# Kernel optimization log

Hardware: AMD Instinct MI355X
Metric: run time of the kernel (lower is better)

Reference implementation:

```python
import jax, jax.numpy as jnp
import numpy as np

B, L, D, H = 2, 128, 256, 256
BASE_LR = 0.01
LR_SHIFT = float(np.log(np.expm1(BASE_LR)))  # log(expm1(base_lr))


def silu_backward(x):
    s = jax.nn.silu(x)
    return s + jax.nn.sigmoid(x) * (1.0 - s)


def decay_matrix(log_g):
    # log_g: [B,L] -> M[b,l,m] = exp(sum_{i=m+1..l} log_g[b,i]) for m<=l, else 0
    n = log_g.shape[1]
    strict = jnp.tril(jnp.ones((n, n), log_g.dtype), -1)
    cum = jnp.cumsum(log_g[:, :, None] * strict, axis=1)
    return jnp.exp(cum) * jnp.tril(jnp.ones((n, n), log_g.dtype))


def setup_inputs():
    key = jax.random.key(0)
    ks = jax.random.split(key, 22)
    p = lambda k, shape: jax.random.normal(k, shape, jnp.float32) * 0.02
    inp = {
        'x': jax.random.normal(ks[0], (B, L, D), jnp.float32),
        'Wq': p(ks[1], (D, D)), 'bq': p(ks[2], (D,)),
        'Wk': p(ks[3], (D, D)), 'bk': p(ks[4], (D,)),
        'Wv': p(ks[5], (D, D)), 'bv': p(ks[6], (D,)),
        'Wlr': p(ks[7], (D, 1)), 'blr': p(ks[8], (1,)),
        'Wm': p(ks[9], (D, 1)), 'bm': p(ks[10], (1,)),
        'Wd': p(ks[11], (D, 1)), 'bd': p(ks[12], (1,)),
        'W1': p(ks[13], (B, H, D)), 'b1': p(ks[14], (B, H)),
        'W2': p(ks[15], (B, D, H)), 'b2': p(ks[16], (B, D)),
        'mW1': p(ks[17], (B, H, D)), 'mb1': p(ks[18], (B, H)),
        'mW2': p(ks[19], (B, D, H)), 'mb2': p(ks[20], (B, D)),
    }
    return inp


def reference(x, Wq, bq, Wk, bk, Wv, bv, Wlr, blr, Wm, bm, Wd, bd,
              W1, b1, W2, b2, mW1, mb1, mW2, mb2):
    query = x @ Wq + bq
    key_ = x @ Wk + bk
    value = x @ Wv + bv

    # forward through fast-weight MLP at current (chunk-start) weights
    Z1 = jnp.einsum('bhd,bld->blh', W1, key_) + b1[:, None, :]
    X2 = jax.nn.silu(Z1)
    Z2 = jnp.einsum('bdh,blh->bld', W2, X2) + b2[:, None, :]

    # per-token gradients of 0.5*||Z2 - value||^2
    grad_Z2 = Z2 - value
    grad_b2 = grad_Z2
    grad_W2 = jnp.einsum('bld,blh->bldh', grad_Z2, X2)
    grad_X2 = jnp.einsum('bld,bdh->blh', grad_Z2, W2)
    grad_Z1 = grad_X2 * silu_backward(Z1)
    grad_b1 = grad_Z1
    grad_W1 = jnp.einsum('blh,bld->blhd', grad_Z1, key_)

    lr = jax.nn.softplus((x @ Wlr).squeeze(-1) + blr + LR_SHIFT)  # [B,L]
    gW1 = grad_W1 * lr[:, :, None, None]
    gb1 = grad_b1 * lr[:, :, None]
    gW2 = grad_W2 * lr[:, :, None, None]
    gb2 = grad_b2 * lr[:, :, None]

    # momentum recurrence (decay-gated linear scan, materialized as LxL matrix)
    fc_mom = (x @ Wm).squeeze(-1) + bm  # [B,L]
    log_mom = -jax.nn.softplus(-fc_mom)
    M = decay_matrix(log_mom)  # [B,L,L]
    mom_cum = jnp.exp(jnp.cumsum(log_mom, axis=1))  # [B,L]

    mgW1 = jnp.einsum('blm,bmhd->blhd', M, gW1) - jnp.einsum('bl,bhd->blhd', mom_cum, mW1)
    mgb1 = jnp.einsum('blm,bmh->blh', M, gb1) - jnp.einsum('bl,bh->blh', mom_cum, mb1)
    mgW2 = jnp.einsum('blm,bmdh->bldh', M, gW2) - jnp.einsum('bl,bdh->bldh', mom_cum, mW2)
    mgb2 = jnp.einsum('blm,bmd->bld', M, gb2) - jnp.einsum('bl,bd->bld', mom_cum, mb2)

    # weight-decay recurrence
    log_wd = -jax.nn.softplus((x @ Wd).squeeze(-1) + bd)  # [B,L]
    Dm = decay_matrix(log_wd)
    wd_cum = jnp.exp(jnp.cumsum(log_wd, axis=1))

    W1p = jnp.einsum('blm,bmhd->blhd', Dm, mgW1) + jnp.einsum('bl,bhd->blhd', wd_cum, W1)
    b1p = jnp.einsum('blm,bmh->blh', Dm, mgb1) + jnp.einsum('bl,bh->blh', wd_cum, b1)
    W2p = jnp.einsum('blm,bmdh->bldh', Dm, mgW2) + jnp.einsum('bl,bdh->bldh', wd_cum, W2)
    b2p = jnp.einsum('blm,bmd->bld', Dm, mgb2) + jnp.einsum('bl,bd->bld', wd_cum, b2)

    # query pass through per-token updated weights
    Zq1 = jnp.einsum('blhd,bld->blh', W1p, query) + b1p
    Zq2 = jnp.einsum('bldh,blh->bld', W2p, jax.nn.silu(Zq1)) + b2p

    return (Zq2,
            W1p[:, -1], b1p[:, -1], W2p[:, -1], b2p[:, -1],
            mgW1[:, -1], mgb1[:, -1], mgW2[:, -1], mgb2[:, -1])
```

## Files before the change

kernel.cpp:

```cpp
#include <hip/hip_runtime.h>
#include <math.h>

constexpr int Bn = 2, Ln = 128, Dn = 256, Hn = 256;

#define LR_SHIFT (-4.6001660040607144f)

constexpr int OFF_Q      = 0;
constexpr int OFF_K      = 65536;
constexpr int OFF_V      = 131072;
constexpr int OFF_X2     = 196608;
constexpr int OFF_GZ1    = 262144;
constexpr int OFF_GZ2    = 327680;
constexpr int OFF_XQ     = 393216;
constexpr int OFF_KT     = 458752;
constexpr int OFF_A      = 524288;
constexpr int OFF_W1T    = 557056;
constexpr int OFF_W2T    = 688128;
constexpr int OFF_MW1T   = 819200;
constexpr int OFF_MW2T   = 950272;
constexpr int OFF_LR     = 1081344;
constexpr int OFF_PM     = 1081600;
constexpr int OFF_PD     = 1081856;
constexpr int OFF_MOMCUM = 1082112;
constexpr int OFF_WDCUM  = 1082368;
constexpr int OFF_C      = 1082624;
constexpr int OFF_LOGM   = 1082880;
constexpr int OFF_LOGWD  = 1083136;
constexpr int OFF_X2T    = 1083392;
constexpr int OFF_U1     = 1148928;
constexpr int OFF_V1     = 1214464;
constexpr int OFF_U2     = 1280000;
constexpr int OFF_V2     = 1345536;
constexpr int OFF_P1     = 1411072;
constexpr int OFF_P2     = OFF_V;

constexpr int OUT_ZQ2  = 0;
constexpr int OUT_W1P  = 65536;
constexpr int OUT_B1P  = 196608;
constexpr int OUT_W2P  = 197120;
constexpr int OUT_B2P  = 328192;
constexpr int OUT_MGW1 = 328704;
constexpr int OUT_MGB1 = 459776;
constexpr int OUT_MGW2 = 460288;
constexpr int OUT_MGB2 = 591360;

struct KParams {
    const float *x;
    const float *Wq, *bq, *Wk, *bk, *Wv, *bv;
    const float *Wlr, *blr, *Wm, *bm, *Wd, *bd;
    const float *W1, *b1, *W2, *b2, *mW1, *mb1, *mW2, *mb2;
    float *out, *ws;
};

__device__ __forceinline__ float softplus_f(float z) {
    return fmaxf(z, 0.0f) + log1pf(expf(-fabsf(z)));
}
__device__ __forceinline__ float4 fma4(float s, const float4 w, float4 a) {
    a.x += s * w.x; a.y += s * w.y; a.z += s * w.z; a.w += s * w.w; return a;
}
__device__ __forceinline__ float silu_f(float z) {
    return z / (1.0f + expf(-z));
}
__device__ __forceinline__ float dsilu_mul(float a, float z) {
    float sg = 1.0f / (1.0f + expf(-z));
    return a * (sg * (1.0f + z * (1.0f - sg)));
}

__device__ __forceinline__ void stage8(const float* __restrict__ src,
                                       float (*xs)[260], int t) {
#pragma unroll
    for (int i = 0; i < 2; ++i) {
        int e = t + i * 256; int tok = e >> 6, kq = e & 63;
        *(float4*)&xs[tok][kq * 4] = *(const float4*)(src + tok * 256 + kq * 4);
    }
}

__device__ __forceinline__ float4 dot256(const float (*xs)[260], int tok,
                                         const float* __restrict__ Wc, int ldw) {
    float4 a = {0, 0, 0, 0};
    for (int k0 = 0; k0 < 256; k0 += 32) {
        float4 wb[32];
#pragma unroll
        for (int kk = 0; kk < 32; ++kk)
            wb[kk] = *(const float4*)(Wc + (k0 + kk) * ldw);
#pragma unroll
        for (int kk = 0; kk < 32; ++kk)
            a = fma4(xs[tok][k0 + kk], wb[kk], a);
    }
    return a;
}

__device__ __forceinline__ void lastw_unit(const KParams& p, float* smem, int t,
                                           int b, int fam, int i0, int j0) {
    const float* ws = p.ws;
    float* wa = smem;
    float* wm = smem + 128;
    float (*LA)[16] = (float (*)[16])(smem + 256);
    float (*LM)[16] = (float (*)[16])(smem + 256 + 2048);
    float (*R)[16]  = (float (*)[16])(smem + 256 + 4096);
    const float* lr = ws + OFF_LR + b * Ln;
    const float* Pm = ws + OFF_PM + b * Ln;
    const float* Arow = ws + OFF_A + (b * Ln + Ln - 1) * Ln;
    if (t < 128) {
        wa[t] = Arow[t] * lr[t];
        wm[t] = expf(Pm[Ln - 1] - Pm[t]) * lr[t];
    }
    const float* left  = ws + (fam == 0 ? OFF_GZ1 : OFF_GZ2) + b * Ln * 256;
    const float* right = ws + (fam == 0 ? OFF_K   : OFF_X2 ) + b * Ln * 256;
    __syncthreads();
#pragma unroll
    for (int i = 0; i < 2; ++i) {
        int e = t + i * 256;
        int m = e >> 2, iq = (e & 3) * 4;
        float4 lv = *(const float4*)(left + m * 256 + i0 + iq);
        float4 rv = *(const float4*)(right + m * 256 + j0 + iq);
        float wam = wa[m], wmm = wm[m];
        LA[m][iq + 0] = wam * lv.x; LA[m][iq + 1] = wam * lv.y;
        LA[m][iq + 2] = wam * lv.z; LA[m][iq + 3] = wam * lv.w;
        LM[m][iq + 0] = wmm * lv.x; LM[m][iq + 1] = wmm * lv.y;
        LM[m][iq + 2] = wmm * lv.z; LM[m][iq + 3] = wmm * lv.w;
        R[m][iq + 0] = rv.x; R[m][iq + 1] = rv.y;
        R[m][iq + 2] = rv.z; R[m][iq + 3] = rv.w;
    }
    __syncthreads();
    int tx = t & 15, ty = t >> 4;
    float accA = 0.0f, accM = 0.0f;
#pragma unroll 4
    for (int m = 0; m < 128; ++m) {
        accA += LA[m][ty] * R[m][tx];
        accM += LM[m][ty] * R[m][tx];
    }
    float c_last  = ws[OFF_C + b * Ln + Ln - 1];
    float wd_last = ws[OFF_WDCUM + b * Ln + Ln - 1];
    float mc_last = ws[OFF_MOMCUM + b * Ln + Ln - 1];
    int i = i0 + ty, j = j0 + tx;
    const float* base1 = (fam == 0 ? p.W1 : p.W2) + b * 65536;
    const float* basem = (fam == 0 ? p.mW1 : p.mW2) + b * 65536;
    float b1v = base1[i * 256 + j], bmv = basem[i * 256 + j];
    int op = (fam == 0 ? OUT_W1P : OUT_W2P) + (b * 256 + i) * 256 + j;
    int om = (fam == 0 ? OUT_MGW1 : OUT_MGW2) + (b * 256 + i) * 256 + j;
    p.out[op] = accA - c_last * bmv + wd_last * b1v;
    p.out[om] = accM - mc_last * bmv;
}

__device__ __forceinline__ void score_unit(const KParams& p, float* smem, int t,
                                           int b, int l0, int srcoff, int btoff,
                                           int poff) {
    const float* ws = p.ws;
    float (*qs)[260] = (float (*)[260])smem;
    stage8(ws + srcoff + (b * 128 + l0) * 256, qs, t);
    __syncthreads();
    int tok = t >> 5, mq = t & 31, m0 = 4 * mq;
    int l = l0 + tok;
    float4 s = dot256(qs, tok, ws + btoff + b * 32768 + m0, 128);
    float4 A4 = *(const float4*)(ws + OFF_A + (b * 128 + l) * 128 + m0);
    float4 L4 = *(const float4*)(ws + OFF_LR + b * 128 + m0);
    float4 pv;
    pv.x = (m0 + 0 <= l) ? A4.x * L4.x * (1.0f + s.x) : 0.0f;
    pv.y = (m0 + 1 <= l) ? A4.y * L4.y * (1.0f + s.y) : 0.0f;
    pv.z = (m0 + 2 <= l) ? A4.z * L4.z * (1.0f + s.z) : 0.0f;
    pv.w = (m0 + 3 <= l) ? A4.w * L4.w * (1.0f + s.w) : 0.0f;
    *(float4*)(p.ws + poff + b * 16384 + l * 128 + m0) = pv;
}

__device__ __forceinline__ void combine_unit(const KParams& p, float* smem, int t,
                                             int b, int l0, int c0, int poff,
                                             int goff, int uoff, int voff,
                                             int dooutsilu, float* dst) {
    const float* ws = p.ws;
    int bl0 = b * 128 + l0;
    float (*ps)[132] = (float (*)[132])smem;
    {
        int tok = t >> 5, mq = t & 31;
        *(float4*)&ps[tok][mq * 4] =
            *(const float4*)(ws + poff + b * 16384 + (l0 + tok) * 128 + mq * 4);
    }
    __syncthreads();
    int tok = t >> 5, q = t & 31;
    int l = l0 + tok;
    int c = c0 + 4 * q;
    float cl  = ws[OFF_C + b * 128 + l];
    float wdc = ws[OFF_WDCUM + b * 128 + l];
    float4 acc = {0, 0, 0, 0};
    const float* G = ws + goff + b * 32768 + c;
    int mmax = l0 + 8;
    int m0 = 0;
    for (; m0 + 16 <= mmax; m0 += 16) {
        float4 gb[16];
#pragma unroll
        for (int kk = 0; kk < 16; ++kk)
            gb[kk] = *(const float4*)(G + (m0 + kk) * 256);
#pragma unroll
        for (int kk = 0; kk < 16; ++kk)
            acc = fma4(ps[tok][m0 + kk], gb[kk], acc);
    }
    for (; m0 < mmax; m0 += 8) {
        float4 gb[8];
#pragma unroll
        for (int kk = 0; kk < 8; ++kk)
            gb[kk] = *(const float4*)(G + (m0 + kk) * 256);
#pragma unroll
        for (int kk = 0; kk < 8; ++kk)
            acc = fma4(ps[tok][m0 + kk], gb[kk], acc);
    }
    float4 u4 = *(const float4*)(ws + uoff + (bl0 + tok) * 256 + c);
    float4 v4 = *(const float4*)(ws + voff + (bl0 + tok) * 256 + c);
    float4 o;
    o.x = acc.x - cl * v4.x + wdc * u4.x;
    o.y = acc.y - cl * v4.y + wdc * u4.y;
    o.z = acc.z - cl * v4.z + wdc * u4.z;
    o.w = acc.w - cl * v4.w + wdc * u4.w;
    if (dooutsilu) {
        o.x = silu_f(o.x); o.y = silu_f(o.y); o.z = silu_f(o.z); o.w = silu_f(o.w);
    }
    *(float4*)(dst + (bl0 + tok) * 256 + c) = o;
}

__global__ __launch_bounds__(256) void phase0_kernel(KParams p) {
    __shared__ float smem[4160];
    int u = blockIdx.x, t = threadIdx.x;
    float* ws = p.ws;
    if (u < 512) {
        int z = u >> 6; int mat = z >> 1; int b = z & 1;
        const float* src; float* dst;
        if (mat == 0)      { src = p.W1  + b * 65536; dst = ws + OFF_W1T  + b * 65536; }
        else if (mat == 1) { src = p.W2  + b * 65536; dst = ws + OFF_W2T  + b * 65536; }
        else if (mat == 2) { src = p.mW1 + b * 65536; dst = ws + OFF_MW1T + b * 65536; }
        else               { src = p.mW2 + b * 65536; dst = ws + OFF_MW2T + b * 65536; }
        float (*tile)[33] = (float (*)[33])smem;
        int tx = t & 31, ty = t >> 5;
        int tid = u & 63;
        int r0 = (tid >> 3) * 32, c0 = (tid & 7) * 32;
        for (int i = 0; i < 32; i += 8)
            tile[ty + i][tx] = src[(r0 + ty + i) * 256 + (c0 + tx)];
        __syncthreads();
        for (int i = 0; i < 32; i += 8)
            dst[(c0 + ty + i) * 256 + (r0 + tx)] = tile[tx][ty + i];
    } else if (u < 704) {
        int v = u - 512; int mat = v >> 6; int r = v & 63;
        int ct = r >> 5, tt = r & 31;
        int bl0 = tt * 8, c0 = ct * 128;
        const float* W    = (mat == 0) ? p.Wq : (mat == 1) ? p.Wk : p.Wv;
        const float* bias = (mat == 0) ? p.bq : (mat == 1) ? p.bk : p.bv;
        int outoff = (mat == 0) ? OFF_Q : (mat == 1) ? OFF_K : OFF_V;
        float (*xs)[260] = (float (*)[260])smem;
        stage8(p.x + bl0 * 256, xs, t);
        __syncthreads();
        int tok = t >> 5, q = t & 31;
        int c = c0 + 4 * q;
        float4 a = dot256(xs, tok, W + c, 256);
        float4 bb = *(const float4*)(bias + c);
        a.x += bb.x; a.y += bb.y; a.z += bb.z; a.w += bb.w;
        *(float4*)(ws + outoff + (bl0 + tok) * 256 + c) = a;
        if (mat == 1) {
            int b = bl0 >> 7, l = (bl0 & 127) + tok;
            float* KT = ws + OFF_KT + b * 32768 + l;
            KT[(c + 0) * 128] = a.x; KT[(c + 1) * 128] = a.y;
            KT[(c + 2) * 128] = a.z; KT[(c + 3) * 128] = a.w;
        }
    } else {
        int blk = u - 704;
        int ln = t & 63, wv = t >> 6;
        int bl = blk * 4 + wv;
        float4 xv = *(const float4*)(p.x + bl * 256 + ln * 4);
        float4 wl = *(const float4*)(p.Wlr + ln * 4);
        float4 wm = *(const float4*)(p.Wm + ln * 4);
        float4 wd = *(const float4*)(p.Wd + ln * 4);
        float s1 = xv.x * wl.x + xv.y * wl.y + xv.z * wl.z + xv.w * wl.w;
        float s2 = xv.x * wm.x + xv.y * wm.y + xv.z * wm.z + xv.w * wm.w;
        float s3 = xv.x * wd.x + xv.y * wd.y + xv.z * wd.z + xv.w * wd.w;
#pragma unroll
        for (int off = 32; off > 0; off >>= 1) {
            s1 += __shfl_xor(s1, off);
            s2 += __shfl_xor(s2, off);
            s3 += __shfl_xor(s3, off);
        }
        if (ln == 0) {
            ws[OFF_LR + bl]    = softplus_f(s1 + p.blr[0] + LR_SHIFT);
            ws[OFF_LOGM + bl]  = -softplus_f(-(s2 + p.bm[0]));
            ws[OFF_LOGWD + bl] = -softplus_f(s3 + p.bd[0]);
        }
    }
}

__global__ __launch_bounds__(256) void phase1_kernel(KParams p) {
    __shared__ float smem[4160];
    int u = blockIdx.x, t = threadIdx.x;
    float* ws = p.ws;
    if (u < 64) {
        int tt = u >> 1, ct = u & 1;
        int bl0 = tt * 8, c0 = ct * 128, b = bl0 >> 7;
        float (*xs)[260] = (float (*)[260])smem;
        stage8(ws + OFF_K + bl0 * 256, xs, t);
        __syncthreads();
        int tok = t >> 5, q = t & 31;
        int c = c0 + 4 * q;
        float4 a = dot256(xs, tok, ws + OFF_W1T + b * 65536 + c, 256);
        float4 bb = *(const float4*)(p.b1 + b * 256 + c);
        float4 z = {a.x + bb.x, a.y + bb.y, a.z + bb.z, a.w + bb.w};
        *(float4*)(ws + OFF_GZ1 + (bl0 + tok) * 256 + c) = z;
        float4 s = {silu_f(z.x), silu_f(z.y), silu_f(z.z), silu_f(z.w)};
        *(float4*)(ws + OFF_X2 + (bl0 + tok) * 256 + c) = s;
        int l = (bl0 & 127) + tok;
        float* X2T = ws + OFF_X2T + b * 32768 + l;
        X2T[(c + 0) * 128] = s.x; X2T[(c + 1) * 128] = s.y;
        X2T[(c + 2) * 128] = s.z; X2T[(c + 3) * 128] = s.w;
    } else if (u < 320) {
        int w = u - 64; int b = w >> 7; int l = w & 127;
        float* sm = smem;
        float* sd = smem + 128;
        float* se = smem + 256;
        if (t < 128) {
            sm[t] = ws[OFF_LOGM + b * Ln + t];
            sd[t] = ws[OFF_LOGWD + b * Ln + t];
        }
        __syncthreads();
        for (int off = 1; off < 128; off <<= 1) {
            float am = 0.0f, ad = 0.0f;
            if (t < 128 && t >= off) { am = sm[t - off]; ad = sd[t - off]; }
            __syncthreads();
            if (t < 128) { sm[t] += am; sd[t] += ad; }
            __syncthreads();
        }
        if (l == 0) {
            if (t < 128) {
                float pm = sm[t], pd = sd[t];
                ws[OFF_PM + b * Ln + t] = pm;
                ws[OFF_PD + b * Ln + t] = pd;
                ws[OFF_MOMCUM + b * Ln + t] = expf(pm);
                ws[OFF_WDCUM + b * Ln + t]  = expf(pd);
                se[t] = expf(pm - pd);
            }
            __syncthreads();
            for (int off = 1; off < 128; off <<= 1) {
                float a = 0.0f;
                if (t < 128 && t >= off) a = se[t - off];
                __syncthreads();
                if (t < 128) se[t] += a;
                __syncthreads();
            }
            if (t < 128) ws[OFF_C + b * Ln + t] = expf(sd[t]) * se[t];
        }
        if (t < 128) {
            int m1 = t;
            float a = 0.0f;
            if (m1 <= l) {
                float pdl = sd[l], pmm1 = sm[m1];
                float s = 0.0f;
                for (int m = m1; m <= l; ++m)
                    s += expf((pdl - sd[m]) + (sm[m] - pmm1));
                a = s;
            }
            ws[OFF_A + (b * Ln + l) * Ln + m1] = a;
        }
    } else {
        int w = u - 320; int mat = w >> 6; int r = w & 63;
        int tt = r >> 1, ct = r & 1;
        int bl0 = tt * 8, c0 = ct * 128, b = bl0 >> 7;
        float (*xs)[260] = (float (*)[260])smem;
        stage8(ws + OFF_Q + bl0 * 256, xs, t);
        __syncthreads();
        int tok = t >> 5, q = t & 31;
        int c = c0 + 4 * q;
        const float* W = ws + (mat ? OFF_MW1T : OFF_W1T) + b * 65536 + c;
        const float* bias = (mat ? p.mb1 : p.b1) + b * 256 + c;
        float4 a = dot256(xs, tok, W, 256);
        float4 bb = *(const float4*)bias;
        a.x += bb.x; a.y += bb.y; a.z += bb.z; a.w += bb.w;
        *(float4*)(ws + (mat ? OFF_V1 : OFF_U1) + (bl0 + tok) * 256 + c) = a;
    }
}

__global__ __launch_bounds__(256) void phase2_kernel(KParams p) {
    __shared__ float smem[4160];
    int u = blockIdx.x, t = threadIdx.x;
    float* ws = p.ws;
    if (u < 64) {
        int tt = u >> 1, ct = u & 1;
        int bl0 = tt * 8, c0 = ct * 128, b = bl0 >> 7;
        float (*xs)[260] = (float (*)[260])smem;
        stage8(ws + OFF_X2 + bl0 * 256, xs, t);
        __syncthreads();
        int tok = t >> 5, q = t & 31;
        int c = c0 + 4 * q;
        float4 a = dot256(xs, tok, ws + OFF_W2T + b * 65536 + c, 256);
        float4 bb = *(const float4*)(p.b2 + b * 256 + c);
        float4 v4 = *(const float4*)(ws + OFF_V + (bl0 + tok) * 256 + c);
        float4 g = {a.x + bb.x - v4.x, a.y + bb.y - v4.y,
                    a.z + bb.z - v4.z, a.w + bb.w - v4.w};
        *(float4*)(ws + OFF_GZ2 + (bl0 + tok) * 256 + c) = g;
    } else {
        int w = u - 64; int b = w >> 4; int l0 = (w & 15) * 8;
        score_unit(p, smem, t, b, l0, OFF_Q, OFF_KT, OFF_P1);
    }
}

__global__ __launch_bounds__(256) void phase3_kernel(KParams p) {
    __shared__ float smem[6400];
    int u = blockIdx.x, t = threadIdx.x;
    float* ws = p.ws;
    if (u < 64) {
        int tt = u >> 1, ct = u & 1;
        int bl0 = tt * 8, c0 = ct * 128, b = bl0 >> 7;
        float (*xs)[260] = (float (*)[260])smem;
        stage8(ws + OFF_GZ2 + bl0 * 256, xs, t);
        __syncthreads();
        int tok = t >> 5, q = t & 31;
        int c = c0 + 4 * q;
        float4 a = dot256(xs, tok, p.W2 + b * 65536 + c, 256);
        float4 z = *(const float4*)(ws + OFF_GZ1 + (bl0 + tok) * 256 + c);
        float4 g = {dsilu_mul(a.x, z.x), dsilu_mul(a.y, z.y),
                    dsilu_mul(a.z, z.z), dsilu_mul(a.w, z.w)};
        *(float4*)(ws + OFF_GZ1 + (bl0 + tok) * 256 + c) = g;
    } else {
        int w = u - 64; int b = w >> 8; int rem = w & 255;
        lastw_unit(p, smem, t, b, 1, (rem >> 4) * 16, (rem & 15) * 16);
    }
}

__global__ __launch_bounds__(256) void phase4_kernel(KParams p) {
    __shared__ float smem[6400];
    int u = blockIdx.x, t = threadIdx.x;
    float* ws = p.ws;
    if (u < 64) {
        int tt = u >> 1, ct = u & 1;
        int b = tt >> 4, l0 = (tt & 15) * 8;
        combine_unit(p, smem, t, b, l0, ct * 128, OFF_P1, OFF_GZ1,
                     OFF_U1, OFF_V1, 1, ws + OFF_XQ);
    } else if (u < 576) {
        int w = u - 64; int b = w >> 8; int rem = w & 255;
        lastw_unit(p, smem, t, b, 0, (rem >> 4) * 16, (rem & 15) * 16);
    } else {
        int b = u - 576;
        float* wa = smem;
        float* wm = smem + 128;
        if (t < 128) {
            wa[t] = ws[OFF_A + (b * Ln + Ln - 1) * Ln + t] * ws[OFF_LR + b * Ln + t];
            wm[t] = expf(ws[OFF_PM + b * Ln + Ln - 1] - ws[OFF_PM + b * Ln + t]) *
                    ws[OFF_LR + b * Ln + t];
        }
        __syncthreads();
        const float* gz1 = ws + OFF_GZ1 + b * Ln * 256;
        const float* gz2 = ws + OFF_GZ2 + b * Ln * 256;
        float sA1 = 0, sM1 = 0, sA2 = 0, sM2 = 0;
        for (int m0 = 0; m0 < 128; m0 += 16) {
            float g1b[16], g2b[16];
#pragma unroll
            for (int kk = 0; kk < 16; ++kk) {
                g1b[kk] = gz1[(m0 + kk) * 256 + t];
                g2b[kk] = gz2[(m0 + kk) * 256 + t];
            }
#pragma unroll
            for (int kk = 0; kk < 16; ++kk) {
                float wam = wa[m0 + kk], wmm = wm[m0 + kk];
                sA1 += wam * g1b[kk]; sM1 += wmm * g1b[kk];
                sA2 += wam * g2b[kk]; sM2 += wmm * g2b[kk];
            }
        }
        float c_last  = ws[OFF_C + b * Ln + Ln - 1];
        float wd_last = ws[OFF_WDCUM + b * Ln + Ln - 1];
        float mc_last = ws[OFF_MOMCUM + b * Ln + Ln - 1];
        p.out[OUT_B1P + b * 256 + t]  = sA1 - c_last * p.mb1[b * 256 + t] + wd_last * p.b1[b * 256 + t];
        p.out[OUT_MGB1 + b * 256 + t] = sM1 - mc_last * p.mb1[b * 256 + t];
        p.out[OUT_B2P + b * 256 + t]  = sA2 - c_last * p.mb2[b * 256 + t] + wd_last * p.b2[b * 256 + t];
        p.out[OUT_MGB2 + b * 256 + t] = sM2 - mc_last * p.mb2[b * 256 + t];
    }
}

__global__ __launch_bounds__(256) void phase5_kernel(KParams p) {
    __shared__ float smem[4160];
    int u = blockIdx.x, t = threadIdx.x;
    float* ws = p.ws;
    if (u < 32) {
        int b = u >> 4; int l0 = (u & 15) * 8;
        score_unit(p, smem, t, b, l0, OFF_XQ, OFF_X2T, OFF_P2);
    } else {
        int w = u - 32; int mat = w >> 6; int r = w & 63;
        int tt = r >> 1, ct = r & 1;
        int bl0 = tt * 8, c0 = ct * 128, b = bl0 >> 7;
        float (*xs)[260] = (float (*)[260])smem;
        stage8(ws + OFF_XQ + bl0 * 256, xs, t);
        __syncthreads();
        int tok = t >> 5, q = t & 31;
        int c = c0 + 4 * q;
        const float* W = ws + (mat ? OFF_MW2T : OFF_W2T) + b * 65536 + c;
        const float* bias = (mat ? p.mb2 : p.b2) + b * 256 + c;
        float4 a = dot256(xs, tok, W, 256);
        float4 bb = *(const float4*)bias;
        a.x += bb.x; a.y += bb.y; a.z += bb.z; a.w += bb.w;
        *(float4*)(ws + (mat ? OFF_V2 : OFF_U2) + (bl0 + tok) * 256 + c) = a;
    }
}

__global__ __launch_bounds__(256) void phase6_kernel(KParams p) {
    __shared__ float smem[1056];
    int u = blockIdx.x, t = threadIdx.x;
    int tt = u >> 1, ct = u & 1;
    int b = tt >> 4, l0 = (tt & 15) * 8;
    combine_unit(p, smem, t, b, l0, ct * 128, OFF_P2, OFF_GZ2,
                 OFF_U2, OFF_V2, 0, p.out + OUT_ZQ2);
}

extern "C" void kernel_launch(void* const* d_in, const int* in_sizes, int n_in,
                              void* d_out, int out_size, void* d_ws, size_t ws_size,
                              hipStream_t stream) {
    KParams p;
    p.x   = (const float*)d_in[0];
    p.Wq  = (const float*)d_in[1];  p.bq  = (const float*)d_in[2];
    p.Wk  = (const float*)d_in[3];  p.bk  = (const float*)d_in[4];
    p.Wv  = (const float*)d_in[5];  p.bv  = (const float*)d_in[6];
    p.Wlr = (const float*)d_in[7];  p.blr = (const float*)d_in[8];
    p.Wm  = (const float*)d_in[9];  p.bm  = (const float*)d_in[10];
    p.Wd  = (const float*)d_in[11]; p.bd  = (const float*)d_in[12];
    p.W1  = (const float*)d_in[13]; p.b1  = (const float*)d_in[14];
    p.W2  = (const float*)d_in[15]; p.b2  = (const float*)d_in[16];
    p.mW1 = (const float*)d_in[17]; p.mb1 = (const float*)d_in[18];
    p.mW2 = (const float*)d_in[19]; p.mb2 = (const float*)d_in[20];
    p.out = (float*)d_out;
    p.ws  = (float*)d_ws;

    phase0_kernel<<<768, 256, 0, stream>>>(p);
    phase1_kernel<<<448, 256, 0, stream>>>(p);
    phase2_kernel<<<96, 256, 0, stream>>>(p);
    phase3_kernel<<<576, 256, 0, stream>>>(p);
    phase4_kernel<<<578, 256, 0, stream>>>(p);
    phase5_kernel<<<160, 256, 0, stream>>>(p);
    phase6_kernel<<<64, 256, 0, stream>>>(p);
}
```

Before: 234.0 us.

## Fuse backward and query-pass phases into fewer kernels, cut launches from seven to four

Merges the grad_Z2 and grad_Z1 computations into one block per 8-token tile, keeping grad_Z2 in shared memory. It also fuses the query-side combine, score, U2/V2 projections and final output into a single per-tile path, which removes the U2/V2/P2 workspace round-trips. That path runs inside the same launch as the last-weight reductions, so two launches and several global-memory passes disappear. The dot256 prefetch batch shrinks from 32 to 16 float4 registers to offset the higher register pressure. The trade-off is fewer blocks for the serial per-tile work, so each block does much more sequential computation.

```diff
diff --git a/kernel.cpp b/kernel.cpp
--- a/kernel.cpp
+++ b/kernel.cpp
@@ -29,10 +29,7 @@
 constexpr int OFF_X2T    = 1083392;
 constexpr int OFF_U1     = 1148928;
 constexpr int OFF_V1     = 1214464;
-constexpr int OFF_U2     = 1280000;
-constexpr int OFF_V2     = 1345536;
 constexpr int OFF_P1     = 1411072;
-constexpr int OFF_P2     = OFF_V;
 
 constexpr int OUT_ZQ2  = 0;
 constexpr int OUT_W1P  = 65536;
@@ -78,13 +75,13 @@
 __device__ __forceinline__ float4 dot256(const float (*xs)[260], int tok,
                                          const float* __restrict__ Wc, int ldw) {
     float4 a = {0, 0, 0, 0};
-    for (int k0 = 0; k0 < 256; k0 += 32) {
-        float4 wb[32];
-#pragma unroll
-        for (int kk = 0; kk < 32; ++kk)
+    for (int k0 = 0; k0 < 256; k0 += 16) {
+        float4 wb[16];
+#pragma unroll
+        for (int kk = 0; kk < 16; ++kk)
             wb[kk] = *(const float4*)(Wc + (k0 + kk) * ldw);
 #pragma unroll
-        for (int kk = 0; kk < 32; ++kk)
+        for (int kk = 0; kk < 16; ++kk)
             a = fma4(xs[tok][k0 + kk], wb[kk], a);
     }
     return a;
@@ -163,27 +160,10 @@
     *(float4*)(p.ws + poff + b * 16384 + l * 128 + m0) = pv;
 }
 
-__device__ __forceinline__ void combine_unit(const KParams& p, float* smem, int t,
-                                             int b, int l0, int c0, int poff,
-                                             int goff, int uoff, int voff,
-                                             int dooutsilu, float* dst) {
-    const float* ws = p.ws;
-    int bl0 = b * 128 + l0;
-    float (*ps)[132] = (float (*)[132])smem;
-    {
-        int tok = t >> 5, mq = t & 31;
-        *(float4*)&ps[tok][mq * 4] =
-            *(const float4*)(ws + poff + b * 16384 + (l0 + tok) * 128 + mq * 4);
-    }
-    __syncthreads();
-    int tok = t >> 5, q = t & 31;
-    int l = l0 + tok;
-    int c = c0 + 4 * q;
-    float cl  = ws[OFF_C + b * 128 + l];
-    float wdc = ws[OFF_WDCUM + b * 128 + l];
+__device__ __forceinline__ float4 pg_dot(const float* __restrict__ G,
+                                         const float* __restrict__ prow,
+                                         int mmax) {
     float4 acc = {0, 0, 0, 0};
-    const float* G = ws + goff + b * 32768 + c;
-    int mmax = l0 + 8;
     int m0 = 0;
     for (; m0 + 16 <= mmax; m0 += 16) {
         float4 gb[16];
@@ -192,7 +172,7 @@
             gb[kk] = *(const float4*)(G + (m0 + kk) * 256);
 #pragma unroll
         for (int kk = 0; kk < 16; ++kk)
-            acc = fma4(ps[tok][m0 + kk], gb[kk], acc);
+            acc = fma4(prow[m0 + kk], gb[kk], acc);
     }
     for (; m0 < mmax; m0 += 8) {
         float4 gb[8];
@@ -201,19 +181,9 @@
             gb[kk] = *(const float4*)(G + (m0 + kk) * 256);
 #pragma unroll
         for (int kk = 0; kk < 8; ++kk)
-            acc = fma4(ps[tok][m0 + kk], gb[kk], acc);
-    }
-    float4 u4 = *(const float4*)(ws + uoff + (bl0 + tok) * 256 + c);
-    float4 v4 = *(const float4*)(ws + voff + (bl0 + tok) * 256 + c);
-    float4 o;
-    o.x = acc.x - cl * v4.x + wdc * u4.x;
-    o.y = acc.y - cl * v4.y + wdc * u4.y;
-    o.z = acc.z - cl * v4.z + wdc * u4.z;
-    o.w = acc.w - cl * v4.w + wdc * u4.w;
-    if (dooutsilu) {
-        o.x = silu_f(o.x); o.y = silu_f(o.y); o.z = silu_f(o.z); o.w = silu_f(o.w);
-    }
-    *(float4*)(dst + (bl0 + tok) * 256 + c) = o;
+            acc = fma4(prow[m0 + kk], gb[kk], acc);
+    }
+    return acc;
 }
 
 __global__ __launch_bounds__(256) void phase0_kernel(KParams p) {
@@ -375,22 +345,47 @@
     __shared__ float smem[4160];
     int u = blockIdx.x, t = threadIdx.x;
     float* ws = p.ws;
-    if (u < 64) {
-        int tt = u >> 1, ct = u & 1;
-        int bl0 = tt * 8, c0 = ct * 128, b = bl0 >> 7;
+    if (u < 32) {
+        int bl0 = u * 8, b = bl0 >> 7;
         float (*xs)[260] = (float (*)[260])smem;
+        float (*gs)[260] = (float (*)[260])(smem + 2080);
         stage8(ws + OFF_X2 + bl0 * 256, xs, t);
         __syncthreads();
         int tok = t >> 5, q = t & 31;
-        int c = c0 + 4 * q;
-        float4 a = dot256(xs, tok, ws + OFF_W2T + b * 65536 + c, 256);
-        float4 bb = *(const float4*)(p.b2 + b * 256 + c);
-        float4 v4 = *(const float4*)(ws + OFF_V + (bl0 + tok) * 256 + c);
-        float4 g = {a.x + bb.x - v4.x, a.y + bb.y - v4.y,
-                    a.z + bb.z - v4.z, a.w + bb.w - v4.w};
-        *(float4*)(ws + OFF_GZ2 + (bl0 + tok) * 256 + c) = g;
+        int c = 4 * q, c2 = c + 128;
+        {
+            const float* W2t = ws + OFF_W2T + b * 65536;
+            float4 a0 = dot256(xs, tok, W2t + c, 256);
+            float4 a1 = dot256(xs, tok, W2t + c2, 256);
+            float4 bb0 = *(const float4*)(p.b2 + b * 256 + c);
+            float4 bb1 = *(const float4*)(p.b2 + b * 256 + c2);
+            float4 v0 = *(const float4*)(ws + OFF_V + (bl0 + tok) * 256 + c);
+            float4 v1 = *(const float4*)(ws + OFF_V + (bl0 + tok) * 256 + c2);
+            float4 g0 = {a0.x + bb0.x - v0.x, a0.y + bb0.y - v0.y,
+                         a0.z + bb0.z - v0.z, a0.w + bb0.w - v0.w};
+            float4 g1 = {a1.x + bb1.x - v1.x, a1.y + bb1.y - v1.y,
+                         a1.z + bb1.z - v1.z, a1.w + bb1.w - v1.w};
+            *(float4*)&gs[tok][c]  = g0;
+            *(float4*)&gs[tok][c2] = g1;
+            *(float4*)(ws + OFF_GZ2 + (bl0 + tok) * 256 + c)  = g0;
+            *(float4*)(ws + OFF_GZ2 + (bl0 + tok) * 256 + c2) = g1;
+        }
+        __syncthreads();
+        {
+            const float* W2n = p.W2 + b * 65536;
+            float4 a0 = dot256(gs, tok, W2n + c, 256);
+            float4 a1 = dot256(gs, tok, W2n + c2, 256);
+            float4 z0 = *(const float4*)(ws + OFF_GZ1 + (bl0 + tok) * 256 + c);
+            float4 z1 = *(const float4*)(ws + OFF_GZ1 + (bl0 + tok) * 256 + c2);
+            float4 g0 = {dsilu_mul(a0.x, z0.x), dsilu_mul(a0.y, z0.y),
+                         dsilu_mul(a0.z, z0.z), dsilu_mul(a0.w, z0.w)};
+            float4 g1 = {dsilu_mul(a1.x, z1.x), dsilu_mul(a1.y, z1.y),
+                         dsilu_mul(a1.z, z1.z), dsilu_mul(a1.w, z1.w)};
+            *(float4*)(ws + OFF_GZ1 + (bl0 + tok) * 256 + c)  = g0;
+            *(float4*)(ws + OFF_GZ1 + (bl0 + tok) * 256 + c2) = g1;
+        }
     } else {
-        int w = u - 64; int b = w >> 4; int l0 = (w & 15) * 8;
+        int w = u - 32; int b = w >> 4; int l0 = (w & 15) * 8;
         score_unit(p, smem, t, b, l0, OFF_Q, OFF_KT, OFF_P1);
     }
 }
@@ -399,39 +394,71 @@
     __shared__ float smem[6400];
     int u = blockIdx.x, t = threadIdx.x;
     float* ws = p.ws;
-    if (u < 64) {
-        int tt = u >> 1, ct = u & 1;
-        int bl0 = tt * 8, c0 = ct * 128, b = bl0 >> 7;
-        float (*xs)[260] = (float (*)[260])smem;
-        stage8(ws + OFF_GZ2 + bl0 * 256, xs, t);
+    if (u < 32) {
+        int b = u >> 4; int l0 = (u & 15) * 8; int bl0 = b * 128 + l0;
+        float (*xqs)[260] = (float (*)[260])smem;
+        float (*ps)[132]  = (float (*)[132])(smem + 2080);
+        {
+            int tok = t >> 5, mq = t & 31;
+            *(float4*)&ps[tok][mq * 4] =
+                *(const float4*)(ws + OFF_P1 + b * 16384 + (l0 + tok) * 128 + mq * 4);
+        }
         __syncthreads();
         int tok = t >> 5, q = t & 31;
-        int c = c0 + 4 * q;
-        float4 a = dot256(xs, tok, p.W2 + b * 65536 + c, 256);
-        float4 z = *(const float4*)(ws + OFF_GZ1 + (bl0 + tok) * 256 + c);
-        float4 g = {dsilu_mul(a.x, z.x), dsilu_mul(a.y, z.y),
-                    dsilu_mul(a.z, z.z), dsilu_mul(a.w, z.w)};
-        *(float4*)(ws + OFF_GZ1 + (bl0 + tok) * 256 + c) = g;
+        int l = l0 + tok;
+        float cl  = ws[OFF_C + b * 128 + l];
+        float wdc = ws[OFF_WDCUM + b * 128 + l];
+        int mmax = l0 + 8;
+#pragma unroll
+        for (int half = 0; half < 2; ++half) {
+            int c = half * 128 + 4 * q;
+            float4 acc = pg_dot(ws + OFF_GZ1 + b * 32768 + c, ps[tok], mmax);
+            float4 u4 = *(const float4*)(ws + OFF_U1 + (bl0 + tok) * 256 + c);
+            float4 v4 = *(const float4*)(ws + OFF_V1 + (bl0 + tok) * 256 + c);
+            float4 o;
+            o.x = silu_f(acc.x - cl * v4.x + wdc * u4.x);
+            o.y = silu_f(acc.y - cl * v4.y + wdc * u4.y);
+            o.z = silu_f(acc.z - cl * v4.z + wdc * u4.z);
+            o.w = silu_f(acc.w - cl * v4.w + wdc * u4.w);
+            *(float4*)&xqs[tok][c] = o;
+        }
+        __syncthreads();
+        {
+            int mq = t & 31, m0 = 4 * mq;
+            float4 s = dot256(xqs, tok, ws + OFF_X2T + b * 32768 + m0, 128);
+            float4 A4 = *(const float4*)(ws + OFF_A + (b * 128 + l) * 128 + m0);
+            float4 L4 = *(const float4*)(ws + OFF_LR + b * 128 + m0);
+            float4 pv;
+            pv.x = (m0 + 0 <= l) ? A4.x * L4.x * (1.0f + s.x) : 0.0f;
+            pv.y = (m0 + 1 <= l) ? A4.y * L4.y * (1.0f + s.y) : 0.0f;
+            pv.z = (m0 + 2 <= l) ? A4.z * L4.z * (1.0f + s.z) : 0.0f;
+            pv.w = (m0 + 3 <= l) ? A4.w * L4.w * (1.0f + s.w) : 0.0f;
+            *(float4*)&ps[tok][m0] = pv;
+        }
+        __syncthreads();
+#pragma unroll
+        for (int half = 0; half < 2; ++half) {
+            int c = half * 128 + 4 * q;
+            float4 uacc = dot256(xqs, tok, ws + OFF_W2T + b * 65536 + c, 256);
+            float4 bb = *(const float4*)(p.b2 + b * 256 + c);
+            uacc.x += bb.x; uacc.y += bb.y; uacc.z += bb.z; uacc.w += bb.w;
+            float4 vacc = dot256(xqs, tok, ws + OFF_MW2T + b * 65536 + c, 256);
+            float4 mb = *(const float4*)(p.mb2 + b * 256 + c);
+            vacc.x += mb.x; vacc.y += mb.y; vacc.z += mb.z; vacc.w += mb.w;
+            float4 acc = pg_dot(ws + OFF_GZ2 + b * 32768 + c, ps[tok], mmax);
+            float4 o;
+            o.x = acc.x - cl * vacc.x + wdc * uacc.x;
+            o.y = acc.y - cl * vacc.y + wdc * uacc.y;
+            o.z = acc.z - cl * vacc.z + wdc * uacc.z;
+            o.w = acc.w - cl * vacc.w + wdc * uacc.w;
+            *(float4*)(p.out + OUT_ZQ2 + (bl0 + tok) * 256 + c) = o;
+        }
+    } else if (u < 1056) {
+        int w = u - 32; int z = w >> 8; int rem = w & 255;
+        int b = z >> 1; int fam = z & 1;
+        lastw_unit(p, smem, t, b, fam, (rem >> 4) * 16, (rem & 15) * 16);
     } else {
-        int w = u - 64; int b = w >> 8; int rem = w & 255;
-        lastw_unit(p, smem, t, b, 1, (rem >> 4) * 16, (rem & 15) * 16);
-    }
-}
-
-__global__ __launch_bounds__(256) void phase4_kernel(KParams p) {
-    __shared__ float smem[6400];
-    int u = blockIdx.x, t = threadIdx.x;
-    float* ws = p.ws;
-    if (u < 64) {
-        int tt = u >> 1, ct = u & 1;
-        int b = tt >> 4, l0 = (tt & 15) * 8;
-        combine_unit(p, smem, t, b, l0, ct * 128, OFF_P1, OFF_GZ1,
-                     OFF_U1, OFF_V1, 1, ws + OFF_XQ);
-    } else if (u < 576) {
-        int w = u - 64; int b = w >> 8; int rem = w & 255;
-        lastw_unit(p, smem, t, b, 0, (rem >> 4) * 16, (rem & 15) * 16);
-    } else {
-        int b = u - 576;
+        int b = u - 1056;
         float* wa = smem;
         float* wm = smem + 128;
         if (t < 128) {
@@ -465,40 +492,6 @@
         p.out[OUT_B2P + b * 256 + t]  = sA2 - c_last * p.mb2[b * 256 + t] + wd_last * p.b2[b * 256 + t];
         p.out[OUT_MGB2 + b * 256 + t] = sM2 - mc_last * p.mb2[b * 256 + t];
     }
-}
-
-__global__ __launch_bounds__(256) void phase5_kernel(KParams p) {
-    __shared__ float smem[4160];
-    int u = blockIdx.x, t = threadIdx.x;
-    float* ws = p.ws;
-    if (u < 32) {
-        int b = u >> 4; int l0 = (u & 15) * 8;
-        score_unit(p, smem, t, b, l0, OFF_XQ, OFF_X2T, OFF_P2);
-    } else {
-        int w = u - 32; int mat = w >> 6; int r = w & 63;
-        int tt = r >> 1, ct = r & 1;
-        int bl0 = tt * 8, c0 = ct * 128, b = bl0 >> 7;
-        float (*xs)[260] = (float (*)[260])smem;
-        stage8(ws + OFF_XQ + bl0 * 256, xs, t);
-        __syncthreads();
-        int tok = t >> 5, q = t & 31;
-        int c = c0 + 4 * q;
-        const float* W = ws + (mat ? OFF_MW2T : OFF_W2T) + b * 65536 + c;
-        const float* bias = (mat ? p.mb2 : p.b2) + b * 256 + c;
-        float4 a = dot256(xs, tok, W, 256);
-        float4 bb = *(const float4*)bias;
-        a.x += bb.x; a.y += bb.y; a.z += bb.z; a.w += bb.w;
-        *(float4*)(ws + (mat ? OFF_V2 : OFF_U2) + (bl0 + tok) * 256 + c) = a;
-    }
-}
-
-__global__ __launch_bounds__(256) void phase6_kernel(KParams p) {
-    __shared__ float smem[1056];
-    int u = blockIdx.x, t = threadIdx.x;
-    int tt = u >> 1, ct = u & 1;
-    int b = tt >> 4, l0 = (tt & 15) * 8;
-    combine_unit(p, smem, t, b, l0, ct * 128, OFF_P2, OFF_GZ2,
-                 OFF_U2, OFF_V2, 0, p.out + OUT_ZQ2);
 }
 
 extern "C" void kernel_launch(void* const* d_in, const int* in_sizes, int n_in,
@@ -521,9 +514,6 @@
 
     phase0_kernel<<<768, 256, 0, stream>>>(p);
     phase1_kernel<<<448, 256, 0, stream>>>(p);
-    phase2_kernel<<<96, 256, 0, stream>>>(p);
-    phase3_kernel<<<576, 256, 0, stream>>>(p);
-    phase4_kernel<<<578, 256, 0, stream>>>(p);
-    phase5_kernel<<<160, 256, 0, stream>>>(p);
-    phase6_kernel<<<64, 256, 0, stream>>>(p);
-}
+    phase2_kernel<<<64, 256, 0, stream>>>(p);
+    phase3_kernel<<<1058, 256, 0, stream>>>(p);
+}
```

Result: faster. 222.4 us (-4.9%).

## Fuse grad_Z2 and grad_Z1 stages into one kernel and merge last-weight passes

Applied to the files above, without the earlier changes.

The two separate kernels that computed grad_Z2 and then grad_Z1 are merged into one block per 8-token group. Each block computes grad_Z2 for all 256 columns, keeps it in shared memory, and immediately computes grad_Z1 from it, which removes one kernel launch and a global round-trip. Both lastw families now run in a single combined kernel, dot256 uses a smaller 16-deep register prefetch, and the P2 scratch buffer is folded into P1. In exchange, the fused stage runs only 32 blocks, so each block does more serial work and the GPU has less parallelism at that point.

```diff
diff --git a/kernel.cpp b/kernel.cpp
--- a/kernel.cpp
+++ b/kernel.cpp
@@ -32,7 +32,6 @@
 constexpr int OFF_U2     = 1280000;
 constexpr int OFF_V2     = 1345536;
 constexpr int OFF_P1     = 1411072;
-constexpr int OFF_P2     = OFF_V;
 
 constexpr int OUT_ZQ2  = 0;
 constexpr int OUT_W1P  = 65536;
@@ -78,13 +77,13 @@
 __device__ __forceinline__ float4 dot256(const float (*xs)[260], int tok,
                                          const float* __restrict__ Wc, int ldw) {
     float4 a = {0, 0, 0, 0};
-    for (int k0 = 0; k0 < 256; k0 += 32) {
-        float4 wb[32];
-#pragma unroll
-        for (int kk = 0; kk < 32; ++kk)
+    for (int k0 = 0; k0 < 256; k0 += 16) {
+        float4 wb[16];
+#pragma unroll
+        for (int kk = 0; kk < 16; ++kk)
             wb[kk] = *(const float4*)(Wc + (k0 + kk) * ldw);
 #pragma unroll
-        for (int kk = 0; kk < 32; ++kk)
+        for (int kk = 0; kk < 16; ++kk)
             a = fma4(xs[tok][k0 + kk], wb[kk], a);
     }
     return a;
@@ -163,6 +162,32 @@
     *(float4*)(p.ws + poff + b * 16384 + l * 128 + m0) = pv;
 }
 
+__device__ __forceinline__ float4 pg_dot(const float* __restrict__ G,
+                                         const float* __restrict__ prow,
+                                         int mmax) {
+    float4 acc = {0, 0, 0, 0};
+    int m0 = 0;
+    for (; m0 + 16 <= mmax; m0 += 16) {
+        float4 gb[16];
+#pragma unroll
+        for (int kk = 0; kk < 16; ++kk)
+            gb[kk] = *(const float4*)(G + (m0 + kk) * 256);
+#pragma unroll
+        for (int kk = 0; kk < 16; ++kk)
+            acc = fma4(prow[m0 + kk], gb[kk], acc);
+    }
+    for (; m0 < mmax; m0 += 8) {
+        float4 gb[8];
+#pragma unroll
+        for (int kk = 0; kk < 8; ++kk)
+            gb[kk] = *(const float4*)(G + (m0 + kk) * 256);
+#pragma unroll
+        for (int kk = 0; kk < 8; ++kk)
+            acc = fma4(prow[m0 + kk], gb[kk], acc);
+    }
+    return acc;
+}
+
 __device__ __forceinline__ void combine_unit(const KParams& p, float* smem, int t,
                                              int b, int l0, int c0, int poff,
                                              int goff, int uoff, int voff,
@@ -181,28 +206,7 @@
     int c = c0 + 4 * q;
     float cl  = ws[OFF_C + b * 128 + l];
     float wdc = ws[OFF_WDCUM + b * 128 + l];
-    float4 acc = {0, 0, 0, 0};
-    const float* G = ws + goff + b * 32768 + c;
-    int mmax = l0 + 8;
-    int m0 = 0;
-    for (; m0 + 16 <= mmax; m0 += 16) {
-        float4 gb[16];
-#pragma unroll
-        for (int kk = 0; kk < 16; ++kk)
-            gb[kk] = *(const float4*)(G + (m0 + kk) * 256);
-#pragma unroll
-        for (int kk = 0; kk < 16; ++kk)
-            acc = fma4(ps[tok][m0 + kk], gb[kk], acc);
-    }
-    for (; m0 < mmax; m0 += 8) {
-        float4 gb[8];
-#pragma unroll
-        for (int kk = 0; kk < 8; ++kk)
-            gb[kk] = *(const float4*)(G + (m0 + kk) * 256);
-#pragma unroll
-        for (int kk = 0; kk < 8; ++kk)
-            acc = fma4(ps[tok][m0 + kk], gb[kk], acc);
-    }
+    float4 acc = pg_dot(ws + goff + b * 32768 + c, ps[tok], l0 + 8);
     float4 u4 = *(const float4*)(ws + uoff + (bl0 + tok) * 256 + c);
     float4 v4 = *(const float4*)(ws + voff + (bl0 + tok) * 256 + c);
     float4 o;
@@ -375,50 +379,52 @@
     __shared__ float smem[4160];
     int u = blockIdx.x, t = threadIdx.x;
     float* ws = p.ws;
-    if (u < 64) {
-        int tt = u >> 1, ct = u & 1;
-        int bl0 = tt * 8, c0 = ct * 128, b = bl0 >> 7;
+    if (u < 32) {
+        int bl0 = u * 8, b = bl0 >> 7;
         float (*xs)[260] = (float (*)[260])smem;
+        float (*gs)[260] = (float (*)[260])(smem + 2080);
         stage8(ws + OFF_X2 + bl0 * 256, xs, t);
         __syncthreads();
         int tok = t >> 5, q = t & 31;
-        int c = c0 + 4 * q;
-        float4 a = dot256(xs, tok, ws + OFF_W2T + b * 65536 + c, 256);
-        float4 bb = *(const float4*)(p.b2 + b * 256 + c);
-        float4 v4 = *(const float4*)(ws + OFF_V + (bl0 + tok) * 256 + c);
-        float4 g = {a.x + bb.x - v4.x, a.y + bb.y - v4.y,
-                    a.z + bb.z - v4.z, a.w + bb.w - v4.w};
-        *(float4*)(ws + OFF_GZ2 + (bl0 + tok) * 256 + c) = g;
+        int c = 4 * q, c2 = c + 128;
+        {
+            const float* W2t = ws + OFF_W2T + b * 65536;
+            float4 a0 = dot256(xs, tok, W2t + c, 256);
+            float4 a1 = dot256(xs, tok, W2t + c2, 256);
+            float4 bb0 = *(const float4*)(p.b2 + b * 256 + c);
+            float4 bb1 = *(const float4*)(p.b2 + b * 256 + c2);
+            float4 v0 = *(const float4*)(ws + OFF_V + (bl0 + tok) * 256 + c);
+            float4 v1 = *(const float4*)(ws + OFF_V + (bl0 + tok) * 256 + c2);
+            float4 g0 = {a0.x + bb0.x - v0.x, a0.y + bb0.y - v0.y,
+                         a0.z + bb0.z - v0.z, a0.w + bb0.w - v0.w};
+            float4 g1 = {a1.x + bb1.x - v1.x, a1.y + bb1.y - v1.y,
+                         a1.z + bb1.z - v1.z, a1.w + bb1.w - v1.w};
+            *(float4*)&gs[tok][c]  = g0;
+            *(float4*)&gs[tok][c2] = g1;
+            *(float4*)(ws + OFF_GZ2 + (bl0 + tok) * 256 + c)  = g0;
+            *(float4*)(ws + OFF_GZ2 + (bl0 + tok) * 256 + c2) = g1;
+        }
+        __syncthreads();
+        {
+            const float* W2n = p.W2 + b * 65536;
+            float4 a0 = dot256(gs, tok, W2n + c, 256);
+            float4 a1 = dot256(gs, tok, W2n + c2, 256);
+            float4 z0 = *(const float4*)(ws + OFF_GZ1 + (bl0 + tok) * 256 + c);
+            float4 z1 = *(const float4*)(ws + OFF_GZ1 + (bl0 + tok) * 256 + c2);
+            float4 g0 = {dsilu_mul(a0.x, z0.x), dsilu_mul(a0.y, z0.y),
+                         dsilu_mul(a0.z, z0.z), dsilu_mul(a0.w, z0.w)};
+            float4 g1 = {dsilu_mul(a1.x, z1.x), dsilu_mul(a1.y, z1.y),
+                         dsilu_mul(a1.z, z1.z), dsilu_mul(a1.w, z1.w)};
+            *(float4*)(ws + OFF_GZ1 + (bl0 + tok) * 256 + c)  = g0;
+            *(float4*)(ws + OFF_GZ1 + (bl0 + tok) * 256 + c2) = g1;
+        }
     } else {
-        int w = u - 64; int b = w >> 4; int l0 = (w & 15) * 8;
+        int w = u - 32; int b = w >> 4; int l0 = (w & 15) * 8;
         score_unit(p, smem, t, b, l0, OFF_Q, OFF_KT, OFF_P1);
     }
 }
 
 __global__ __launch_bounds__(256) void phase3_kernel(KParams p) {
-    __shared__ float smem[6400];
-    int u = blockIdx.x, t = threadIdx.x;
-    float* ws = p.ws;
-    if (u < 64) {
-        int tt = u >> 1, ct = u & 1;
-        int bl0 = tt * 8, c0 = ct * 128, b = bl0 >> 7;
-        float (*xs)[260] = (float (*)[260])smem;
-        stage8(ws + OFF_GZ2 + bl0 * 256, xs, t);
-        __syncthreads();
-        int tok = t >> 5, q = t & 31;
-        int c = c0 + 4 * q;
-        float4 a = dot256(xs, tok, p.W2 + b * 65536 + c, 256);
-        float4 z = *(const float4*)(ws + OFF_GZ1 + (bl0 + tok) * 256 + c);
-        float4 g = {dsilu_mul(a.x, z.x), dsilu_mul(a.y, z.y),
-                    dsilu_mul(a.z, z.z), dsilu_mul(a.w, z.w)};
-        *(float4*)(ws + OFF_GZ1 + (bl0 + tok) * 256 + c) = g;
-    } else {
-        int w = u - 64; int b = w >> 8; int rem = w & 255;
-        lastw_unit(p, smem, t, b, 1, (rem >> 4) * 16, (rem & 15) * 16);
-    }
-}
-
-__global__ __launch_bounds__(256) void phase4_kernel(KParams p) {
     __shared__ float smem[6400];
     int u = blockIdx.x, t = threadIdx.x;
     float* ws = p.ws;
@@ -427,11 +433,12 @@
         int b = tt >> 4, l0 = (tt & 15) * 8;
         combine_unit(p, smem, t, b, l0, ct * 128, OFF_P1, OFF_GZ1,
                      OFF_U1, OFF_V1, 1, ws + OFF_XQ);
-    } else if (u < 576) {
-        int w = u - 64; int b = w >> 8; int rem = w & 255;
-        lastw_unit(p, smem, t, b, 0, (rem >> 4) * 16, (rem & 15) * 16);
+    } else if (u < 1088) {
+        int w = u - 64; int z = w >> 8; int rem = w & 255;
+        int b = z >> 1; int fam = z & 1;
+        lastw_unit(p, smem, t, b, fam, (rem >> 4) * 16, (rem & 15) * 16);
     } else {
-        int b = u - 576;
+        int b = u - 1088;
         float* wa = smem;
         float* wm = smem + 128;
         if (t < 128) {
@@ -467,13 +474,13 @@
     }
 }
 
-__global__ __launch_bounds__(256) void phase5_kernel(KParams p) {
+__global__ __launch_bounds__(256) void phase4_kernel(KParams p) {
     __shared__ float smem[4160];
     int u = blockIdx.x, t = threadIdx.x;
     float* ws = p.ws;
     if (u < 32) {
         int b = u >> 4; int l0 = (u & 15) * 8;
-        score_unit(p, smem, t, b, l0, OFF_XQ, OFF_X2T, OFF_P2);
+        score_unit(p, smem, t, b, l0, OFF_XQ, OFF_X2T, OFF_P1);
     } else {
         int w = u - 32; int mat = w >> 6; int r = w & 63;
         int tt = r >> 1, ct = r & 1;
@@ -492,12 +499,12 @@
     }
 }
 
-__global__ __launch_bounds__(256) void phase6_kernel(KParams p) {
+__global__ __launch_bounds__(256) void phase5_kernel(KParams p) {
     __shared__ float smem[1056];
     int u = blockIdx.x, t = threadIdx.x;
     int tt = u >> 1, ct = u & 1;
     int b = tt >> 4, l0 = (tt & 15) * 8;
-    combine_unit(p, smem, t, b, l0, ct * 128, OFF_P2, OFF_GZ2,
+    combine_unit(p, smem, t, b, l0, ct * 128, OFF_P1, OFF_GZ2,
                  OFF_U2, OFF_V2, 0, p.out + OUT_ZQ2);
 }
 
@@ -521,9 +528,8 @@
 
     phase0_kernel<<<768, 256, 0, stream>>>(p);
     phase1_kernel<<<448, 256, 0, stream>>>(p);
-    phase2_kernel<<<96, 256, 0, stream>>>(p);
-    phase3_kernel<<<576, 256, 0, stream>>>(p);
-    phase4_kernel<<<578, 256, 0, stream>>>(p);
-    phase5_kernel<<<160, 256, 0, stream>>>(p);
-    phase6_kernel<<<64, 256, 0, stream>>>(p);
-}
+    phase2_kernel<<<64, 256, 0, stream>>>(p);
+    phase3_kernel<<<1090, 256, 0, stream>>>(p);
+    phase4_kernel<<<160, 256, 0, stream>>>(p);
+    phase5_kernel<<<64, 256, 0, stream>>>(p);
+}
```

New measurement: 206.7 us. 1.13x faster.
